# Kernel tuning notes

Measured on AMD Instinct MI355X. Metric: run time of the kernel, lower is better.

Reference implementation:

```python
import jax, jax.numpy as jnp
import numpy as np

N = 7          # num nodes == conv1 in_channels (PyG: x=None -> node indices, in_channels=num_nodes)
H = 16         # hidden channels (hardcoded in the module)
R = 64         # num_relations
C = 8          # out_channels
E = 8_000_000  # num edges


def setup_inputs() -> dict:
    key = jax.random.key(0)
    ks = jax.random.split(key, 7)
    return dict(
        x=jax.random.normal(ks[0], (N, N), jnp.float32),  # ignored: forward passes None to conv1
        edge_index=jax.random.randint(ks[1], (2, E), 0, N, dtype=jnp.int32),
        edge_type=jax.random.randint(ks[2], (E,), 0, R, dtype=jnp.int32),
        W1=jax.random.normal(ks[3], (R, N, H), jnp.float32) / np.sqrt(N).astype(np.float32),
        root1=jax.random.normal(ks[4], (N, H), jnp.float32) / np.sqrt(N).astype(np.float32),
        b1=jnp.zeros((H,), jnp.float32),
        W2=jax.random.normal(ks[5], (R, H, C), jnp.float32) / np.sqrt(H).astype(np.float32),
        root2=jax.random.normal(ks[6], (H, C), jnp.float32) / np.sqrt(H).astype(np.float32),
        b2=jnp.zeros((C,), jnp.float32),
    )


def _rel_mean_norm(dst, edge_type):
    # FastRGCNConv aggr='mean': 1 / max(#in-edges of dst with the same relation, 1), per edge.
    comb = dst * R + edge_type                                    # [E] combined (node, rel) id
    counts = jax.ops.segment_sum(jnp.ones_like(comb, jnp.float32), comb,
                                 num_segments=N * R)              # [N*R]
    return 1.0 / jnp.maximum(counts[comb], 1.0)                   # [E]


def reference(x, edge_index, edge_type, W1, root1, b1, W2, root2, b2):
    src, dst = edge_index[0], edge_index[1]
    norm = _rel_mean_norm(dst, edge_type)                         # [E]

    # layer 1: x is None -> message = W1[edge_type, src] (embedding per relation);
    # root weight acts as an embedding root1[arange(N)] = root1.
    msg1 = W1[edge_type, src] * norm[:, None]                     # [E,H]
    h = jax.ops.segment_sum(msg1, dst, num_segments=N) + root1 + b1
    h = jax.nn.relu(h)                                            # [N,H]

    # layer 2: compute all per-(node, relation) transforms once (N is tiny),
    # then gather per edge — same math as per-edge bmm, avoids [E,H,C] temp.
    hr = jnp.einsum('nh,rhc->nrc', h, W2)                         # [N,R,C]
    msg2 = hr[src, edge_type] * norm[:, None]                     # [E,C]
    out = jax.ops.segment_sum(msg2, dst, num_segments=N) + h @ root2 + b2
    return jax.nn.log_softmax(out, axis=1)                        # [N,C]
```

## Files before the change

### kernel.cpp

```cpp
#include <hip/hip_runtime.h>
#include <hip/hip_bf16.h>

#define NN 7
#define HH 16
#define RR 64
#define CC 8
#define NBINS (NN * RR * NN)

#define HIST_BLOCK 1024
#define HIST_GRID  256
#define NT (HIST_GRID * HIST_BLOCK)

__global__ __launch_bounds__(HIST_BLOCK) void rgcn_hist(
    const int* __restrict__ src, const int* __restrict__ dst,
    const int* __restrict__ et, int E, int* __restrict__ part) {
    __shared__ int bins[NBINS];
    for (int i = threadIdx.x; i < NBINS; i += HIST_BLOCK) bins[i] = 0;
    __syncthreads();

    const int tid = blockIdx.x * HIST_BLOCK + threadIdx.x;
    const int E4 = E >> 2;
    const int4* s4 = reinterpret_cast<const int4*>(src);
    const int4* d4 = reinterpret_cast<const int4*>(dst);
    const int4* t4 = reinterpret_cast<const int4*>(et);

    for (int base = tid; base < E4; base += 4 * NT) {
        int4 S[4], D[4], T[4];
#pragma unroll
        for (int k = 0; k < 4; ++k) {
            int idx = base + k * NT;
            int cl = idx < E4 ? idx : (E4 - 1);
            S[k] = s4[cl];
            D[k] = d4[cl];
            T[k] = t4[cl];
        }
#pragma unroll
        for (int k = 0; k < 4; ++k) {
            const int add = (base + k * NT < E4) ? 1 : 0;
            atomicAdd(&bins[D[k].x * (RR * NN) + T[k].x * NN + S[k].x], add);
            atomicAdd(&bins[D[k].y * (RR * NN) + T[k].y * NN + S[k].y], add);
            atomicAdd(&bins[D[k].z * (RR * NN) + T[k].z * NN + S[k].z], add);
            atomicAdd(&bins[D[k].w * (RR * NN) + T[k].w * NN + S[k].w], add);
        }
    }
    for (int e = (E4 << 2) + tid; e < E; e += NT) {
        atomicAdd(&bins[dst[e] * (RR * NN) + et[e] * NN + src[e]], 1);
    }

    __syncthreads();
    int* myslice = part + blockIdx.x * NBINS;
    for (int i2 = threadIdx.x; i2 < NBINS; i2 += HIST_BLOCK)
        myslice[i2] = bins[i2];
}

__global__ __launch_bounds__(256) void rgcn_reduce(
    const int* __restrict__ part, int* __restrict__ gbins) {
    __shared__ int acc[4][64];
    const int lane = threadIdx.x & 63;
    const int chunk = threadIdx.x >> 6;
    const int bin = blockIdx.x * 64 + lane;

    int s = 0;
    const int p0 = chunk * (HIST_GRID / 4);
#pragma unroll 8
    for (int k = 0; k < HIST_GRID / 4; ++k)
        s += part[(p0 + k) * NBINS + bin];
    acc[chunk][lane] = s;
    __syncthreads();
    if (chunk == 0)
        gbins[bin] = acc[0][lane] + acc[1][lane] + acc[2][lane] + acc[3][lane];
}

__global__ __launch_bounds__(1024) void rgcn_finish(
    const int* __restrict__ gbins,
    const float* __restrict__ W1,
    const float* __restrict__ root1,
    const float* __restrict__ b1,
    const float* __restrict__ W2,
    const float* __restrict__ root2,
    const float* __restrict__ b2,
    float* __restrict__ out) {
    __shared__ float cntf[NN][RR][NN];
    __shared__ float w1s[RR * NN * HH];
    __shared__ float w2s[RR * HH * CC];
    __shared__ float p1[NN][HH][4];
    __shared__ float h[NN][HH];
    __shared__ float hr[NN][RR][CC];
    __shared__ float p2[NN][CC][8];
    __shared__ float o[NN][CC];

    const int t = threadIdx.x;
    const int BD = 1024;
    const float4* W1v = reinterpret_cast<const float4*>(W1);
    for (int i = t; i < RR * NN * HH / 4; i += BD)
        reinterpret_cast<float4*>(w1s)[i] = W1v[i];
    const float4* W2v = reinterpret_cast<const float4*>(W2);
    for (int i = t; i < RR * HH * CC / 4; i += BD)
        reinterpret_cast<float4*>(w2s)[i] = W2v[i];
    for (int i = t; i < NN * RR; i += BD) {
        int n = i / RR, r = i % RR;
        const int* gb = gbins + n * (RR * NN) + r * NN;
        int c[NN];
        int tot = 0;
#pragma unroll
        for (int s = 0; s < NN; ++s) { c[s] = gb[s]; tot += c[s]; }
        float inv = 1.0f / (float)(tot > 0 ? tot : 1);
#pragma unroll
        for (int s = 0; s < NN; ++s) cntf[n][r][s] = (float)c[s] * inv;
    }
    __syncthreads();

    for (int i = t; i < NN * HH * 4; i += BD) {
        int n = i >> 6;
        int j = (i >> 2) & (HH - 1);
        int q = i & 3;
        float acc = 0.0f;
        for (int r = q * 16; r < q * 16 + 16; ++r)
            for (int s = 0; s < NN; ++s)
                acc = fmaf(cntf[n][r][s], w1s[(r * NN + s) * HH + j], acc);
        p1[n][j][q] = acc;
    }
    __syncthreads();
    for (int i = t; i < NN * HH; i += BD) {
        int n = i / HH, j = i % HH;
        float acc = root1[n * HH + j] + b1[j] +
                    p1[n][j][0] + p1[n][j][1] + p1[n][j][2] + p1[n][j][3];
        h[n][j] = fmaxf(acc, 0.0f);
    }
    __syncthreads();

    for (int i = t; i < NN * RR * CC; i += BD) {
        int s = i / (RR * CC);
        int rem = i % (RR * CC);
        int r = rem / CC, c = rem % CC;
        float acc = 0.0f;
        for (int j = 0; j < HH; ++j)
            acc = fmaf(h[s][j], w2s[(r * HH + j) * CC + c], acc);
        hr[s][r][c] = acc;
    }
    __syncthreads();

    for (int i = t; i < NN * CC * 8; i += BD) {
        int n = i >> 6;
        int c = (i >> 3) & (CC - 1);
        int q = i & 7;
        float acc = 0.0f;
        for (int r = q * 8; r < q * 8 + 8; ++r)
            for (int s = 0; s < NN; ++s)
                acc = fmaf(cntf[n][r][s], hr[s][r][c], acc);
        if (q == 0) {
            for (int j = 0; j < HH; ++j)
                acc = fmaf(h[n][j], root2[j * CC + c], acc);
            acc += b2[c];
        }
        p2[n][c][q] = acc;
    }
    __syncthreads();
    for (int i = t; i < NN * CC; i += BD) {
        int n = i / CC, c = i % CC;
        float acc = 0.0f;
        for (int q = 0; q < 8; ++q) acc += p2[n][c][q];
        o[n][c] = acc;
    }
    __syncthreads();

    if (t < NN) {
        float m = -1e30f;
        for (int c = 0; c < CC; ++c) m = fmaxf(m, o[t][c]);
        float sum = 0.0f;
        for (int c = 0; c < CC; ++c) sum += __expf(o[t][c] - m);
        float lse = m + __logf(sum);
        for (int c = 0; c < CC; ++c) out[t * CC + c] = o[t][c] - lse;
    }
}

extern "C" void kernel_launch(void* const* d_in, const int* in_sizes, int n_in,
                              void* d_out, int out_size, void* d_ws, size_t ws_size,
                              hipStream_t stream) {
    const int* edge_index = (const int*)d_in[1];
    const int* edge_type  = (const int*)d_in[2];
    const float* W1    = (const float*)d_in[3];
    const float* root1 = (const float*)d_in[4];
    const float* b1    = (const float*)d_in[5];
    const float* W2    = (const float*)d_in[6];
    const float* root2 = (const float*)d_in[7];
    const float* b2    = (const float*)d_in[8];
    float* out = (float*)d_out;

    const int E = in_sizes[2];
    const int* src = edge_index;
    const int* dst = edge_index + E;

    int* part  = (int*)d_ws;
    int* gbins = part + HIST_GRID * NBINS;

    rgcn_hist<<<HIST_GRID, HIST_BLOCK, 0, stream>>>(src, dst, edge_type, E, part);
    rgcn_reduce<<<49, 256, 0, stream>>>(part, gbins);
    rgcn_finish<<<1, 1024, 0, stream>>>(gbins, W1, root1, b1, W2, root2, b2, out);
}
```

Measured before the change: 37.80 us.

## Fuse histogram, reduce and finish into one kernel with atomic grid sync

Merges the three launches into a single persistent kernel. Blocks publish their partial histograms, sync through global atomic counters, and the first 49 blocks reduce them. The last reducing block, found by a ticket counter, runs the tiny GNN finish stage reading W1/W2 from global memory rather than staging them in shared. The histogram loop also staggers load phases between alternate wavefronts. This removes two launch gaps at the cost of spin-waits, which assume all 256 blocks are co-resident, and a reset protocol for the ready flag between calls.

Result: slower. 80.25 us (+112.3%).

```diff
diff --git a/kernel.cpp b/kernel.cpp
--- a/kernel.cpp
+++ b/kernel.cpp
@@ -10,93 +10,135 @@
 #define HIST_BLOCK 1024
 #define HIST_GRID  256
 #define NT (HIST_GRID * HIST_BLOCK)
-
-__global__ __launch_bounds__(HIST_BLOCK) void rgcn_hist(
+#define RED_BLOCKS 49
+#define MAGIC 0x13579BDF
+
+#define C_CNT1  0
+#define C_CNT2  16
+#define C_READY 32
+
+#define PHASE(START)                                                         \
+    {                                                                        \
+        const int base_ = tid + (START);                                     \
+        int4 S[4], D[4], T[4];                                               \
+        _Pragma("unroll")                                                    \
+        for (int k = 0; k < 4; ++k) {                                        \
+            int idx = base_ + k * NT;                                        \
+            int cl = idx < E4 ? idx : (E4 - 1);                              \
+            S[k] = s4[cl]; D[k] = d4[cl]; T[k] = t4[cl];                     \
+        }                                                                    \
+        _Pragma("unroll")                                                    \
+        for (int k = 0; k < 4; ++k) {                                        \
+            const int add = (base_ + k * NT < E4) ? 1 : 0;                   \
+            atomicAdd(&bins[D[k].x * (RR * NN) + T[k].x * NN + S[k].x], add);\
+            atomicAdd(&bins[D[k].y * (RR * NN) + T[k].y * NN + S[k].y], add);\
+            atomicAdd(&bins[D[k].z * (RR * NN) + T[k].z * NN + S[k].z], add);\
+            atomicAdd(&bins[D[k].w * (RR * NN) + T[k].w * NN + S[k].w], add);\
+        }                                                                    \
+    }
+
+__global__ __launch_bounds__(HIST_BLOCK) void rgcn_fused(
     const int* __restrict__ src, const int* __restrict__ dst,
-    const int* __restrict__ et, int E, int* __restrict__ part) {
-    __shared__ int bins[NBINS];
-    for (int i = threadIdx.x; i < NBINS; i += HIST_BLOCK) bins[i] = 0;
-    __syncthreads();
-
-    const int tid = blockIdx.x * HIST_BLOCK + threadIdx.x;
-    const int E4 = E >> 2;
-    const int4* s4 = reinterpret_cast<const int4*>(src);
-    const int4* d4 = reinterpret_cast<const int4*>(dst);
-    const int4* t4 = reinterpret_cast<const int4*>(et);
-
-    for (int base = tid; base < E4; base += 4 * NT) {
-        int4 S[4], D[4], T[4];
-#pragma unroll
-        for (int k = 0; k < 4; ++k) {
-            int idx = base + k * NT;
-            int cl = idx < E4 ? idx : (E4 - 1);
-            S[k] = s4[cl];
-            D[k] = d4[cl];
-            T[k] = t4[cl];
-        }
-#pragma unroll
-        for (int k = 0; k < 4; ++k) {
-            const int add = (base + k * NT < E4) ? 1 : 0;
-            atomicAdd(&bins[D[k].x * (RR * NN) + T[k].x * NN + S[k].x], add);
-            atomicAdd(&bins[D[k].y * (RR * NN) + T[k].y * NN + S[k].y], add);
-            atomicAdd(&bins[D[k].z * (RR * NN) + T[k].z * NN + S[k].z], add);
-            atomicAdd(&bins[D[k].w * (RR * NN) + T[k].w * NN + S[k].w], add);
-        }
-    }
-    for (int e = (E4 << 2) + tid; e < E; e += NT) {
-        atomicAdd(&bins[dst[e] * (RR * NN) + et[e] * NN + src[e]], 1);
-    }
-
-    __syncthreads();
-    int* myslice = part + blockIdx.x * NBINS;
-    for (int i2 = threadIdx.x; i2 < NBINS; i2 += HIST_BLOCK)
-        myslice[i2] = bins[i2];
-}
-
-__global__ __launch_bounds__(256) void rgcn_reduce(
-    const int* __restrict__ part, int* __restrict__ gbins) {
-    __shared__ int acc[4][64];
-    const int lane = threadIdx.x & 63;
-    const int chunk = threadIdx.x >> 6;
-    const int bin = blockIdx.x * 64 + lane;
-
-    int s = 0;
-    const int p0 = chunk * (HIST_GRID / 4);
-#pragma unroll 8
-    for (int k = 0; k < HIST_GRID / 4; ++k)
-        s += part[(p0 + k) * NBINS + bin];
-    acc[chunk][lane] = s;
-    __syncthreads();
-    if (chunk == 0)
-        gbins[bin] = acc[0][lane] + acc[1][lane] + acc[2][lane] + acc[3][lane];
-}
-
-__global__ __launch_bounds__(1024) void rgcn_finish(
-    const int* __restrict__ gbins,
+    const int* __restrict__ et, int E,
     const float* __restrict__ W1,
     const float* __restrict__ root1,
     const float* __restrict__ b1,
     const float* __restrict__ W2,
     const float* __restrict__ root2,
     const float* __restrict__ b2,
-    float* __restrict__ out) {
+    float* __restrict__ out,
+    int* __restrict__ part, int* __restrict__ gbins, int* __restrict__ ctrl) {
+    __shared__ int   bins[NBINS];
     __shared__ float cntf[NN][RR][NN];
-    __shared__ float w1s[RR * NN * HH];
-    __shared__ float w2s[RR * HH * CC];
     __shared__ float p1[NN][HH][4];
     __shared__ float h[NN][HH];
     __shared__ float hr[NN][RR][CC];
     __shared__ float p2[NN][CC][8];
     __shared__ float o[NN][CC];
+    __shared__ int   lastflag;
 
     const int t = threadIdx.x;
-    const int BD = 1024;
-    const float4* W1v = reinterpret_cast<const float4*>(W1);
-    for (int i = t; i < RR * NN * HH / 4; i += BD)
-        reinterpret_cast<float4*>(w1s)[i] = W1v[i];
-    const float4* W2v = reinterpret_cast<const float4*>(W2);
-    for (int i = t; i < RR * HH * CC / 4; i += BD)
-        reinterpret_cast<float4*>(w2s)[i] = W2v[i];
+    const int b = blockIdx.x;
+
+    if (b == 0 && t == 0) {
+        __hip_atomic_store(&ctrl[C_CNT1], 0, __ATOMIC_RELAXED, __HIP_MEMORY_SCOPE_AGENT);
+        __hip_atomic_store(&ctrl[C_CNT2], 0, __ATOMIC_RELAXED, __HIP_MEMORY_SCOPE_AGENT);
+        __hip_atomic_store(&ctrl[C_READY], MAGIC, __ATOMIC_RELEASE, __HIP_MEMORY_SCOPE_AGENT);
+    }
+
+    for (int i = t; i < NBINS; i += HIST_BLOCK) bins[i] = 0;
+    __syncthreads();
+
+    const int tid = b * HIST_BLOCK + t;
+    const int E4 = E >> 2;
+    const int4* s4 = reinterpret_cast<const int4*>(src);
+    const int4* d4 = reinterpret_cast<const int4*>(dst);
+    const int4* t4 = reinterpret_cast<const int4*>(et);
+
+    if (E4 > 0) {
+        const int first = ((t >> 6) & 1) ? (4 * NT) : 0;
+        for (int off = 0; off < E4; off += 8 * NT) {
+            PHASE(off + first)
+            PHASE(off + (4 * NT) - first)
+        }
+    }
+    for (int e = (E4 << 2) + tid; e < E; e += NT) {
+        atomicAdd(&bins[dst[e] * (RR * NN) + et[e] * NN + src[e]], 1);
+    }
+    __syncthreads();
+
+    int4* slice4 = reinterpret_cast<int4*>(part + b * NBINS);
+    const int4* bins4 = reinterpret_cast<const int4*>(bins);
+    for (int i = t; i < NBINS / 4; i += HIST_BLOCK) slice4[i] = bins4[i];
+    __syncthreads();
+
+    if (t == 0) {
+        while (__hip_atomic_load(&ctrl[C_READY], __ATOMIC_ACQUIRE,
+                                 __HIP_MEMORY_SCOPE_AGENT) != MAGIC)
+            __builtin_amdgcn_s_sleep(8);
+        __threadfence();
+        __hip_atomic_fetch_add(&ctrl[C_CNT1], 1, __ATOMIC_ACQ_REL,
+                               __HIP_MEMORY_SCOPE_AGENT);
+    }
+    if (b >= RED_BLOCKS) return;
+
+    if (t == 0) {
+        while (__hip_atomic_load(&ctrl[C_CNT1], __ATOMIC_ACQUIRE,
+                                 __HIP_MEMORY_SCOPE_AGENT) < HIST_GRID)
+            __builtin_amdgcn_s_sleep(8);
+    }
+    __syncthreads();
+    __threadfence();
+
+    {
+        const int binl = t & 63;
+        const int chunk = t >> 6;
+        const int gbin = b * 64 + binl;
+        int s = 0;
+#pragma unroll
+        for (int k = 0; k < 16; ++k)
+            s += part[(chunk * 16 + k) * NBINS + gbin];
+        bins[chunk * 64 + binl] = s;
+    }
+    __syncthreads();
+    if (t < 64) {
+        int tot = 0;
+#pragma unroll
+        for (int c = 0; c < 16; ++c) tot += bins[c * 64 + t];
+        gbins[b * 64 + t] = tot;
+    }
+    __threadfence();
+    __syncthreads();
+    if (t == 0) {
+        int old = __hip_atomic_fetch_add(&ctrl[C_CNT2], 1, __ATOMIC_ACQ_REL,
+                                         __HIP_MEMORY_SCOPE_AGENT);
+        lastflag = (old == RED_BLOCKS - 1) ? 1 : 0;
+    }
+    __syncthreads();
+    if (!lastflag) return;
+    __threadfence();
+
+    const int BD = HIST_BLOCK;
     for (int i = t; i < NN * RR; i += BD) {
         int n = i / RR, r = i % RR;
         const int* gb = gbins + n * (RR * NN) + r * NN;
@@ -117,7 +159,7 @@
         float acc = 0.0f;
         for (int r = q * 16; r < q * 16 + 16; ++r)
             for (int s = 0; s < NN; ++s)
-                acc = fmaf(cntf[n][r][s], w1s[(r * NN + s) * HH + j], acc);
+                acc = fmaf(cntf[n][r][s], W1[(r * NN + s) * HH + j], acc);
         p1[n][j][q] = acc;
     }
     __syncthreads();
@@ -135,7 +177,7 @@
         int r = rem / CC, c = rem % CC;
         float acc = 0.0f;
         for (int j = 0; j < HH; ++j)
-            acc = fmaf(h[s][j], w2s[(r * HH + j) * CC + c], acc);
+            acc = fmaf(h[s][j], W2[(r * HH + j) * CC + c], acc);
         hr[s][r][c] = acc;
     }
     __syncthreads();
@@ -172,6 +214,10 @@
         float lse = m + __logf(sum);
         for (int c = 0; c < CC; ++c) out[t * CC + c] = o[t][c] - lse;
     }
+    __syncthreads();
+    if (t == 0)
+        __hip_atomic_store(&ctrl[C_READY], 0, __ATOMIC_RELEASE,
+                           __HIP_MEMORY_SCOPE_AGENT);
 }
 
 extern "C" void kernel_launch(void* const* d_in, const int* in_sizes, int n_in,
@@ -193,8 +239,9 @@
 
     int* part  = (int*)d_ws;
     int* gbins = part + HIST_GRID * NBINS;
-
-    rgcn_hist<<<HIST_GRID, HIST_BLOCK, 0, stream>>>(src, dst, edge_type, E, part);
-    rgcn_reduce<<<49, 256, 0, stream>>>(part, gbins);
-    rgcn_finish<<<1, 1024, 0, stream>>>(gbins, W1, root1, b1, W2, root2, b2, out);
+    int* ctrl  = gbins + NBINS;
+
+    rgcn_fused<<<HIST_GRID, HIST_BLOCK, 0, stream>>>(
+        src, dst, edge_type, E, W1, root1, b1, W2, root2, b2, out,
+        part, gbins, ctrl);
 }
```
